# Kernel tuning notes

Hardware: AMD Instinct MI355X
Metric: run time of the kernel (lower is better)

The kernel has to match this reference:

```python
import math
import jax, jax.numpy as jnp
import numpy as np

NUM_HEADS = 8
C_HIDDEN = 32
C_Q = 64
C_KV = 64
INF = 1.0e9


def setup_inputs() -> dict:
    key = jax.random.key(0)
    ks = jax.random.split(key, 8)
    B, S, Q, KV = 1, 128, 256, 256
    H, D = NUM_HEADS, C_HIDDEN
    input_q = jax.random.normal(ks[0], (B, S, Q, C_Q), dtype=jnp.float32)
    input_kv = jax.random.normal(ks[1], (B, S, KV, C_KV), dtype=jnp.float32)
    mask = jnp.ones((B, S, 1, 1, KV), dtype=jnp.float32)
    bias = jax.random.normal(ks[2], (B, 1, H, Q, KV), dtype=jnp.float32)
    # Glorot-ish init for projections
    wq = jax.random.normal(ks[3], (C_Q, H * D), dtype=jnp.float32) * (1.0 / math.sqrt(C_Q))
    wk = jax.random.normal(ks[4], (C_KV, H * D), dtype=jnp.float32) * (1.0 / math.sqrt(C_KV))
    wv = jax.random.normal(ks[5], (C_KV, H * D), dtype=jnp.float32) * (1.0 / math.sqrt(C_KV))
    wo = jax.random.normal(ks[6], (H * D, C_Q), dtype=jnp.float32) * (1.0 / math.sqrt(H * D))
    bo = jnp.zeros((C_Q,), dtype=jnp.float32)
    return {"input_q": input_q, "input_kv": input_kv, "mask": mask, "bias": bias,
            "wq": wq, "wk": wk, "wv": wv, "wo": wo, "bo": bo}


def _split_heads(x):
    # [..., L, H*D] -> [..., H, L, D]
    *lead, L, HD = x.shape
    x = x.reshape(*lead, L, NUM_HEADS, C_HIDDEN)
    return jnp.swapaxes(x, -2, -3)


def reference(input_q, input_kv, mask, bias, wq, wk, wv, wo, bo):
    q = _split_heads(input_q @ wq)   # [B,S,H,Q,D]
    k = _split_heads(input_kv @ wk)  # [B,S,H,KV,D]
    v = _split_heads(input_kv @ wv)  # [B,S,H,KV,D]
    scaling = 1.0 / math.sqrt(C_HIDDEN)
    a = jnp.einsum("bshqd,bshkd->bshqk", q * scaling, k)
    a = a + (mask - 1.0) * INF + bias
    a = jax.nn.softmax(a, axis=-1)
    o = jnp.einsum("bshqk,bshkd->bshqd", a, v)
    o = jnp.swapaxes(o, -2, -3)  # [B,S,Q,H,D]
    o = o.reshape(o.shape[:-2] + (NUM_HEADS * C_HIDDEN,))
    return o @ wo + bo
```

## Files before the change

kernel.cpp:

```cpp
#include <hip/hip_runtime.h>

typedef __bf16 bf16_t;
typedef __bf16 bf16x4_t __attribute__((ext_vector_type(4)));
typedef __bf16 bf16x8 __attribute__((ext_vector_type(8)));
typedef float f32x4 __attribute__((ext_vector_type(4)));

#define NH 8
#define DH 32
#define QL 256
#define KL 256
#define CIN 64
#define HD 256

__device__ __forceinline__ bf16_t f2bf(float x) { return (bf16_t)x; }

__device__ __forceinline__ f32x4 mfma16(bf16x8 a, bf16x8 b, f32x4 c) {
    return __builtin_amdgcn_mfma_f32_16x16x32_bf16(a, b, c, 0, 0, 0);
}

__launch_bounds__(256)
__global__ void pack_w(const float* __restrict__ Wq, const float* __restrict__ Wk,
                       const float* __restrict__ Wv, const float* __restrict__ Wo,
                       bf16_t* __restrict__ WqF, bf16_t* __restrict__ WkF,
                       bf16_t* __restrict__ WvF, bf16_t* __restrict__ WoF) {
    const int h = blockIdx.x;
    const int tid = threadIdx.x, lane = tid & 63, w = tid >> 6;
    const int quad = lane >> 4, l16 = lane & 15;
    if (w < 3) {
        const float* __restrict__ W = (w == 0) ? Wq : (w == 1 ? Wk : Wv);
        bf16_t* __restrict__ F = (w == 0) ? WqF : (w == 1 ? WkF : WvF);
#pragma unroll
        for (int nt = 0; nt < 2; ++nt)
#pragma unroll
            for (int ks = 0; ks < 2; ++ks) {
                bf16x8 f;
#pragma unroll
                for (int j = 0; j < 8; ++j)
                    f[j] = f2bf(W[(ks * 32 + quad * 8 + j) * HD + h * DH + nt * 16 + l16]);
                *(bf16x8*)&F[(size_t)((h * 4 + nt * 2 + ks) * 512) + lane * 8] = f;
            }
    } else {
#pragma unroll
        for (int nt = 0; nt < 4; ++nt) {
            bf16x8 f;
#pragma unroll
            for (int j = 0; j < 8; ++j)
                f[j] = f2bf(Wo[(h * DH + quad * 8 + j) * CIN + nt * 16 + l16]);
            *(bf16x8*)&WoF[(size_t)((h * 4 + nt) * 512) + lane * 8] = f;
        }
    }
}

__launch_bounds__(256, 3)
__global__ void fused_sb(const float* __restrict__ Xq, const float* __restrict__ Xkv,
                         const float* __restrict__ Mask, const float* __restrict__ Bias,
                         const bf16_t* __restrict__ WqF, const bf16_t* __restrict__ WkF,
                         const bf16_t* __restrict__ WvF, const bf16_t* __restrict__ WoF,
                         const float* __restrict__ Bo, float* __restrict__ Out) {
    const int b = blockIdx.x;
    const int s = b & 127;
    const int qq = (b >> 7) & 3, hg = b >> 9;
    const int tid = threadIdx.x, lane = tid & 63, w = tid >> 6;
    const int quad = lane >> 4, l16 = lane & 15;
    const int tg = qq * 4 + w;
    const f32x4 vzero = {0.f, 0.f, 0.f, 0.f};

    __shared__ __attribute__((aligned(16))) bf16_t sK[KL * 32];
    __shared__ __attribute__((aligned(16))) bf16_t sVT[DH][264];
    __shared__ __attribute__((aligned(16))) bf16_t sPT[4][16][72];
    __shared__ __attribute__((aligned(16))) float sMask[KL];

    if (tid < 64) {
        const f32x4 m4 = *(const f32x4*)&Mask[s * KL + tid * 4];
        f32x4 mm;
#pragma unroll
        for (int j = 0; j < 4; ++j) mm[j] = (m4[j] - 1.0f) * 1.0e9f;
        *(f32x4*)&sMask[tid * 4] = mm;
    }

    bf16x8 xk[4][2];
#pragma unroll
    for (int t = 0; t < 4; ++t) {
        const int row = (w * 4 + t) * 16 + l16;
        const float* src = &Xkv[(size_t)(s * QL + row) * CIN];
#pragma unroll
        for (int ks = 0; ks < 2; ++ks) {
            const f32x4 lo = *(const f32x4*)&src[ks * 32 + quad * 8];
            const f32x4 hi = *(const f32x4*)&src[ks * 32 + quad * 8 + 4];
            bf16x8 f;
#pragma unroll
            for (int j = 0; j < 4; ++j) { f[j] = f2bf(lo[j]); f[4 + j] = f2bf(hi[j]); }
            xk[t][ks] = f;
        }
    }
    bf16x8 xq[2];
    {
        const int row = tg * 16 + l16;
        const float* src = &Xq[(size_t)(s * QL + row) * CIN];
#pragma unroll
        for (int ks = 0; ks < 2; ++ks) {
            const f32x4 lo = *(const f32x4*)&src[ks * 32 + quad * 8];
            const f32x4 hi = *(const f32x4*)&src[ks * 32 + quad * 8 + 4];
            bf16x8 f;
#pragma unroll
            for (int j = 0; j < 4; ++j) {
                f[j] = f2bf(lo[j] * 0.17677669529663687f);
                f[4 + j] = f2bf(hi[j] * 0.17677669529663687f);
            }
            xq[ks] = f;
        }
    }

    auto projK = [&](int h) {
        bf16x8 bk[2][2];
#pragma unroll
        for (int nt = 0; nt < 2; ++nt)
#pragma unroll
            for (int ks = 0; ks < 2; ++ks)
                bk[nt][ks] = *(const bf16x8*)&WkF[(size_t)((h * 4 + nt * 2 + ks) * 512) + lane * 8];
#pragma unroll
        for (int t = 0; t < 4; ++t) {
            const int r0 = (w * 4 + t) * 16 + quad * 4;
#pragma unroll
            for (int nt = 0; nt < 2; ++nt) {
                f32x4 c = mfma16(xk[t][0], bk[nt][0], vzero);
                c = mfma16(xk[t][1], bk[nt][1], c);
                const int chS = ((nt * 2 + (l16 >> 3)) ^ quad) << 3;
#pragma unroll
                for (int r = 0; r < 4; ++r)
                    sK[(r0 + r) * 32 + chS + (l16 & 7)] = f2bf(c[r]);
            }
        }
    };
    auto projV = [&](int h) {
        bf16x8 bv[2][2];
#pragma unroll
        for (int nt = 0; nt < 2; ++nt)
#pragma unroll
            for (int ks = 0; ks < 2; ++ks)
                bv[nt][ks] = *(const bf16x8*)&WvF[(size_t)((h * 4 + nt * 2 + ks) * 512) + lane * 8];
#pragma unroll
        for (int t = 0; t < 4; ++t) {
            const int c0 = (w * 4 + t) * 16 + quad * 4;
#pragma unroll
            for (int nt = 0; nt < 2; ++nt) {
                f32x4 c = mfma16(xk[t][0], bv[nt][0], vzero);
                c = mfma16(xk[t][1], bv[nt][1], c);
                bf16x4_t p4;
#pragma unroll
                for (int r = 0; r < 4; ++r) p4[r] = f2bf(c[r]);
                *(bf16x4_t*)&sVT[nt * 16 + l16][c0] = p4;
            }
        }
    };
    auto projQ = [&](int h) -> bf16x8 {
        bf16x8 bq[2][2];
#pragma unroll
        for (int nt = 0; nt < 2; ++nt)
#pragma unroll
            for (int ks = 0; ks < 2; ++ks)
                bq[nt][ks] = *(const bf16x8*)&WqF[(size_t)((h * 4 + nt * 2 + ks) * 512) + lane * 8];
#pragma unroll
        for (int nt = 0; nt < 2; ++nt) {
            f32x4 c = mfma16(xq[0], bq[nt][0], vzero);
            c = mfma16(xq[1], bq[nt][1], c);
#pragma unroll
            for (int r = 0; r < 4; ++r) sPT[w][quad * 4 + r][nt * 16 + l16] = f2bf(c[r]);
        }
        return *(const bf16x8*)&sPT[w][l16][quad * 8];
    };

    f32x4 acc[4];
#pragma unroll
    for (int nt = 0; nt < 4; ++nt) acc[nt] = vzero;

    f32x4 sv[16];
    {
        const float* bb = &Bias[(size_t)(hg * 4 * QL + tg * 16 + l16) * KL];
#pragma unroll
        for (int ct = 0; ct < 16; ++ct) sv[ct] = *(const f32x4*)&bb[ct * 16 + quad * 4];
    }
    projK(hg * 4);
    projV(hg * 4);
    bf16x8 qfr = projQ(hg * 4);
    __syncthreads();

#pragma unroll 1
    for (int hh = 0; hh < 4; ++hh) {
        const int h = hg * 4 + hh;

#pragma unroll
        for (int ct = 0; ct < 16; ++ct) {
            const int row = ct * 16 + l16;
            const int chS = (quad ^ ((l16 >> 2) & 3)) << 3;
            const bf16x8 ak = *(const bf16x8*)&sK[row * 32 + chS];
            sv[ct] = mfma16(ak, qfr, sv[ct]);
        }

        __syncthreads();

        if (hh < 3) projK(h + 1);

#pragma unroll
        for (int ct = 0; ct < 16; ++ct)
            sv[ct] += *(const f32x4*)&sMask[ct * 16 + quad * 4];
        f32x4 vmx = sv[0];
#pragma unroll
        for (int ct = 1; ct < 16; ++ct)
#pragma unroll
            for (int r = 0; r < 4; ++r) vmx[r] = fmaxf(vmx[r], sv[ct][r]);
        float mx = fmaxf(fmaxf(vmx[0], vmx[1]), fmaxf(vmx[2], vmx[3]));
        mx = fmaxf(mx, __shfl_xor(mx, 16, 64));
        mx = fmaxf(mx, __shfl_xor(mx, 32, 64));
        f32x4 vsum = vzero;
#pragma unroll
        for (int ct = 0; ct < 16; ++ct)
#pragma unroll
            for (int r = 0; r < 4; ++r) {
                const float e = __expf(sv[ct][r] - mx);
                sv[ct][r] = e;
                vsum[r] += e;
            }
        float sum = (vsum[0] + vsum[1]) + (vsum[2] + vsum[3]);
        sum += __shfl_xor(sum, 16, 64);
        sum += __shfl_xor(sum, 32, 64);
        const float rs = 1.0f / sum;

        f32x4 o0 = vzero, o1 = vzero;
#pragma unroll
        for (int c = 0; c < 4; ++c) {
#pragma unroll
            for (int cc = 0; cc < 4; ++cc) {
                const int ct = c * 4 + cc;
                bf16x4_t pv;
#pragma unroll
                for (int r = 0; r < 4; ++r) pv[r] = f2bf(sv[ct][r] * rs);
                *(bf16x4_t*)&sPT[w][l16][cc * 16 + quad * 4] = pv;
            }
#pragma unroll
            for (int ks = 0; ks < 2; ++ks) {
                const bf16x8 ap = *(const bf16x8*)&sPT[w][l16][ks * 32 + quad * 8];
                const int cs = c * 2 + ks;
                const bf16x8 v0 = *(const bf16x8*)&sVT[l16][cs * 32 + quad * 8];
                const bf16x8 v1 = *(const bf16x8*)&sVT[16 + l16][cs * 32 + quad * 8];
                o0 = mfma16(ap, v0, o0);
                o1 = mfma16(ap, v1, o1);
            }
        }

        __syncthreads();

        if (hh < 3) projV(h + 1);

        {
            bf16x8 bwo[4];
#pragma unroll
            for (int nt = 0; nt < 4; ++nt)
                bwo[nt] = *(const bf16x8*)&WoF[(size_t)((h * 4 + nt) * 512) + lane * 8];
#pragma unroll
            for (int r = 0; r < 4; ++r) {
                sPT[w][quad * 4 + r][l16] = f2bf(o0[r]);
                sPT[w][quad * 4 + r][16 + l16] = f2bf(o1[r]);
            }
            const bf16x8 af = *(const bf16x8*)&sPT[w][l16][quad * 8];
#pragma unroll
            for (int nt = 0; nt < 4; ++nt) acc[nt] = mfma16(af, bwo[nt], acc[nt]);
        }

        if (hh < 3) {
            qfr = projQ(h + 1);
            const float* bb = &Bias[(size_t)((h + 1) * QL + tg * 16 + l16) * KL];
#pragma unroll
            for (int ct = 0; ct < 16; ++ct) sv[ct] = *(const f32x4*)&bb[ct * 16 + quad * 4];
        }
    }

    const int orow = s * QL + tg * 16 + quad * 4;
#pragma unroll
    for (int nt = 0; nt < 4; ++nt) {
        const float bo = (hg == 0) ? Bo[nt * 16 + l16] : 0.0f;
#pragma unroll
        for (int r = 0; r < 4; ++r)
            atomicAdd(&Out[(size_t)(orow + r) * CIN + nt * 16 + l16], acc[nt][r] + bo);
    }
}

extern "C" void kernel_launch(void* const* d_in, const int* in_sizes, int n_in,
                              void* d_out, int out_size, void* d_ws, size_t ws_size,
                              hipStream_t stream) {
    const float* Xq   = (const float*)d_in[0];
    const float* Xkv  = (const float*)d_in[1];
    const float* Mask = (const float*)d_in[2];
    const float* Bias = (const float*)d_in[3];
    const float* Wq   = (const float*)d_in[4];
    const float* Wk   = (const float*)d_in[5];
    const float* Wv   = (const float*)d_in[6];
    const float* Wo   = (const float*)d_in[7];
    const float* Bo   = (const float*)d_in[8];
    float* Out = (float*)d_out;

    bf16_t* WqF = (bf16_t*)d_ws;
    bf16_t* WkF = WqF + 16384;
    bf16_t* WvF = WkF + 16384;
    bf16_t* WoF = WvF + 16384;

    pack_w<<<dim3(NH), 256, 0, stream>>>(Wq, Wk, Wv, Wo, WqF, WkF, WvF, WoF);
    hipMemsetAsync(d_out, 0, (size_t)out_size, stream);
    fused_sb<<<dim3(1024), 256, 0, stream>>>(Xq, Xkv, Mask, Bias,
                                             WqF, WkF, WvF, WoF, Bo, Out);
}
```

Before: 158.9 us.

## Process all heads per block, two heads interleaved, replacing atomics with plain stores

The head-group split across blocks is removed, so each block now covers all 8 heads for its (s, q-tile) and the grid halves to 512 blocks. Heads are handled in pairs with double-buffered K/V shared memory, which gives two independent MFMA and softmax chains to interleave for more ILP. Because one block owns a full output tile, the memset and the atomicAdd output accumulation are replaced by direct stores. The cost is more registers and LDS per block, lower occupancy (launch bound 2 instead of 3), and half as many blocks, which may under-fill the GPU's compute units and repeats the X loads less often but spends more serial time per block.

```diff
diff --git a/kernel.cpp b/kernel.cpp
--- a/kernel.cpp
+++ b/kernel.cpp
@@ -51,22 +51,21 @@
     }
 }
 
-__launch_bounds__(256, 3)
-__global__ void fused_sb(const float* __restrict__ Xq, const float* __restrict__ Xkv,
+__launch_bounds__(256, 2)
+__global__ void fused_g2(const float* __restrict__ Xq, const float* __restrict__ Xkv,
                          const float* __restrict__ Mask, const float* __restrict__ Bias,
                          const bf16_t* __restrict__ WqF, const bf16_t* __restrict__ WkF,
                          const bf16_t* __restrict__ WvF, const bf16_t* __restrict__ WoF,
                          const float* __restrict__ Bo, float* __restrict__ Out) {
     const int b = blockIdx.x;
-    const int s = b & 127;
-    const int qq = (b >> 7) & 3, hg = b >> 9;
+    const int s = b & 127, qq = b >> 7;
     const int tid = threadIdx.x, lane = tid & 63, w = tid >> 6;
     const int quad = lane >> 4, l16 = lane & 15;
     const int tg = qq * 4 + w;
     const f32x4 vzero = {0.f, 0.f, 0.f, 0.f};
 
-    __shared__ __attribute__((aligned(16))) bf16_t sK[KL * 32];
-    __shared__ __attribute__((aligned(16))) bf16_t sVT[DH][264];
+    __shared__ __attribute__((aligned(16))) bf16_t sK[2][KL * 32];
+    __shared__ __attribute__((aligned(16))) bf16_t sVT[2][DH][264];
     __shared__ __attribute__((aligned(16))) bf16_t sPT[4][16][72];
     __shared__ __attribute__((aligned(16))) float sMask[KL];
 
@@ -111,7 +110,7 @@
         }
     }
 
-    auto projK = [&](int h) {
+    auto projK = [&](int h, int buf) {
         bf16x8 bk[2][2];
 #pragma unroll
         for (int nt = 0; nt < 2; ++nt)
@@ -128,11 +127,11 @@
                 const int chS = ((nt * 2 + (l16 >> 3)) ^ quad) << 3;
 #pragma unroll
                 for (int r = 0; r < 4; ++r)
-                    sK[(r0 + r) * 32 + chS + (l16 & 7)] = f2bf(c[r]);
+                    sK[buf][(r0 + r) * 32 + chS + (l16 & 7)] = f2bf(c[r]);
             }
         }
     };
-    auto projV = [&](int h) {
+    auto projV = [&](int h, int buf) {
         bf16x8 bv[2][2];
 #pragma unroll
         for (int nt = 0; nt < 2; ++nt)
@@ -149,7 +148,7 @@
                 bf16x4_t p4;
 #pragma unroll
                 for (int r = 0; r < 4; ++r) p4[r] = f2bf(c[r]);
-                *(bf16x4_t*)&sVT[nt * 16 + l16][c0] = p4;
+                *(bf16x4_t*)&sVT[buf][nt * 16 + l16][c0] = p4;
             }
         }
     };
@@ -174,59 +173,89 @@
 #pragma unroll
     for (int nt = 0; nt < 4; ++nt) acc[nt] = vzero;
 
-    f32x4 sv[16];
-    {
-        const float* bb = &Bias[(size_t)(hg * 4 * QL + tg * 16 + l16) * KL];
-#pragma unroll
-        for (int ct = 0; ct < 16; ++ct) sv[ct] = *(const f32x4*)&bb[ct * 16 + quad * 4];
-    }
-    projK(hg * 4);
-    projV(hg * 4);
-    bf16x8 qfr = projQ(hg * 4);
+    f32x4 sv[2][16];
+#pragma unroll
+    for (int u = 0; u < 2; ++u) {
+        const float* bb = &Bias[(size_t)(u * QL + tg * 16 + l16) * KL];
+#pragma unroll
+        for (int ct = 0; ct < 16; ++ct) sv[u][ct] = *(const f32x4*)&bb[ct * 16 + quad * 4];
+    }
+    projK(0, 0);
+    projK(1, 1);
+    projV(0, 0);
+    projV(1, 1);
+    bf16x8 qfr0 = projQ(0);
+    bf16x8 qfr1 = projQ(1);
     __syncthreads();
 
 #pragma unroll 1
-    for (int hh = 0; hh < 4; ++hh) {
-        const int h = hg * 4 + hh;
+    for (int i = 0; i < 4; ++i) {
+        const int h0 = 2 * i, h1 = 2 * i + 1;
 
 #pragma unroll
         for (int ct = 0; ct < 16; ++ct) {
             const int row = ct * 16 + l16;
             const int chS = (quad ^ ((l16 >> 2) & 3)) << 3;
-            const bf16x8 ak = *(const bf16x8*)&sK[row * 32 + chS];
-            sv[ct] = mfma16(ak, qfr, sv[ct]);
+            const bf16x8 ak0 = *(const bf16x8*)&sK[0][row * 32 + chS];
+            const bf16x8 ak1 = *(const bf16x8*)&sK[1][row * 32 + chS];
+            sv[0][ct] = mfma16(ak0, qfr0, sv[0][ct]);
+            sv[1][ct] = mfma16(ak1, qfr1, sv[1][ct]);
         }
 
         __syncthreads();
 
-        if (hh < 3) projK(h + 1);
-
+        if (i < 3) {
+            projK(h0 + 2, 0);
+            projK(h1 + 2, 1);
+        }
+
+        f32x4 vmx0, vmx1;
+        {
+            const f32x4 m0 = *(const f32x4*)&sMask[0 * 16 + quad * 4];
+            sv[0][0] += m0;
+            sv[1][0] += m0;
+            vmx0 = sv[0][0];
+            vmx1 = sv[1][0];
+        }
+#pragma unroll
+        for (int ct = 1; ct < 16; ++ct) {
+            const f32x4 mm = *(const f32x4*)&sMask[ct * 16 + quad * 4];
+            sv[0][ct] += mm;
+            sv[1][ct] += mm;
+#pragma unroll
+            for (int r = 0; r < 4; ++r) {
+                vmx0[r] = fmaxf(vmx0[r], sv[0][ct][r]);
+                vmx1[r] = fmaxf(vmx1[r], sv[1][ct][r]);
+            }
+        }
+        float mx0 = fmaxf(fmaxf(vmx0[0], vmx0[1]), fmaxf(vmx0[2], vmx0[3]));
+        float mx1 = fmaxf(fmaxf(vmx1[0], vmx1[1]), fmaxf(vmx1[2], vmx1[3]));
+        mx0 = fmaxf(mx0, __shfl_xor(mx0, 16, 64));
+        mx1 = fmaxf(mx1, __shfl_xor(mx1, 16, 64));
+        mx0 = fmaxf(mx0, __shfl_xor(mx0, 32, 64));
+        mx1 = fmaxf(mx1, __shfl_xor(mx1, 32, 64));
+        f32x4 vs0 = vzero, vs1 = vzero;
 #pragma unroll
         for (int ct = 0; ct < 16; ++ct)
-            sv[ct] += *(const f32x4*)&sMask[ct * 16 + quad * 4];
-        f32x4 vmx = sv[0];
-#pragma unroll
-        for (int ct = 1; ct < 16; ++ct)
-#pragma unroll
-            for (int r = 0; r < 4; ++r) vmx[r] = fmaxf(vmx[r], sv[ct][r]);
-        float mx = fmaxf(fmaxf(vmx[0], vmx[1]), fmaxf(vmx[2], vmx[3]));
-        mx = fmaxf(mx, __shfl_xor(mx, 16, 64));
-        mx = fmaxf(mx, __shfl_xor(mx, 32, 64));
-        f32x4 vsum = vzero;
-#pragma unroll
-        for (int ct = 0; ct < 16; ++ct)
 #pragma unroll
             for (int r = 0; r < 4; ++r) {
-                const float e = __expf(sv[ct][r] - mx);
-                sv[ct][r] = e;
-                vsum[r] += e;
-            }
-        float sum = (vsum[0] + vsum[1]) + (vsum[2] + vsum[3]);
-        sum += __shfl_xor(sum, 16, 64);
-        sum += __shfl_xor(sum, 32, 64);
-        const float rs = 1.0f / sum;
-
-        f32x4 o0 = vzero, o1 = vzero;
+                const float e0 = __expf(sv[0][ct][r] - mx0);
+                const float e1 = __expf(sv[1][ct][r] - mx1);
+                sv[0][ct][r] = e0;
+                sv[1][ct][r] = e1;
+                vs0[r] += e0;
+                vs1[r] += e1;
+            }
+        float sum0 = (vs0[0] + vs0[1]) + (vs0[2] + vs0[3]);
+        float sum1 = (vs1[0] + vs1[1]) + (vs1[2] + vs1[3]);
+        sum0 += __shfl_xor(sum0, 16, 64);
+        sum1 += __shfl_xor(sum1, 16, 64);
+        sum0 += __shfl_xor(sum0, 32, 64);
+        sum1 += __shfl_xor(sum1, 32, 64);
+        const float rs0 = 1.0f / sum0;
+        const float rs1 = 1.0f / sum1;
+
+        f32x4 o00 = vzero, o01 = vzero, o10 = vzero, o11 = vzero;
 #pragma unroll
         for (int c = 0; c < 4; ++c) {
 #pragma unroll
@@ -234,54 +263,93 @@
                 const int ct = c * 4 + cc;
                 bf16x4_t pv;
 #pragma unroll
-                for (int r = 0; r < 4; ++r) pv[r] = f2bf(sv[ct][r] * rs);
+                for (int r = 0; r < 4; ++r) pv[r] = f2bf(sv[0][ct][r] * rs0);
                 *(bf16x4_t*)&sPT[w][l16][cc * 16 + quad * 4] = pv;
             }
 #pragma unroll
             for (int ks = 0; ks < 2; ++ks) {
                 const bf16x8 ap = *(const bf16x8*)&sPT[w][l16][ks * 32 + quad * 8];
                 const int cs = c * 2 + ks;
-                const bf16x8 v0 = *(const bf16x8*)&sVT[l16][cs * 32 + quad * 8];
-                const bf16x8 v1 = *(const bf16x8*)&sVT[16 + l16][cs * 32 + quad * 8];
-                o0 = mfma16(ap, v0, o0);
-                o1 = mfma16(ap, v1, o1);
+                const bf16x8 v0 = *(const bf16x8*)&sVT[0][l16][cs * 32 + quad * 8];
+                const bf16x8 v1 = *(const bf16x8*)&sVT[0][16 + l16][cs * 32 + quad * 8];
+                o00 = mfma16(ap, v0, o00);
+                o01 = mfma16(ap, v1, o01);
+            }
+#pragma unroll
+            for (int cc = 0; cc < 4; ++cc) {
+                const int ct = c * 4 + cc;
+                bf16x4_t pv;
+#pragma unroll
+                for (int r = 0; r < 4; ++r) pv[r] = f2bf(sv[1][ct][r] * rs1);
+                *(bf16x4_t*)&sPT[w][l16][cc * 16 + quad * 4] = pv;
+            }
+#pragma unroll
+            for (int ks = 0; ks < 2; ++ks) {
+                const bf16x8 ap = *(const bf16x8*)&sPT[w][l16][ks * 32 + quad * 8];
+                const int cs = c * 2 + ks;
+                const bf16x8 v0 = *(const bf16x8*)&sVT[1][l16][cs * 32 + quad * 8];
+                const bf16x8 v1 = *(const bf16x8*)&sVT[1][16 + l16][cs * 32 + quad * 8];
+                o10 = mfma16(ap, v0, o10);
+                o11 = mfma16(ap, v1, o11);
             }
         }
 
         __syncthreads();
 
-        if (hh < 3) projV(h + 1);
+        if (i < 3) {
+            projV(h0 + 2, 0);
+            projV(h1 + 2, 1);
+        }
 
         {
             bf16x8 bwo[4];
 #pragma unroll
             for (int nt = 0; nt < 4; ++nt)
-                bwo[nt] = *(const bf16x8*)&WoF[(size_t)((h * 4 + nt) * 512) + lane * 8];
+                bwo[nt] = *(const bf16x8*)&WoF[(size_t)((h0 * 4 + nt) * 512) + lane * 8];
 #pragma unroll
             for (int r = 0; r < 4; ++r) {
-                sPT[w][quad * 4 + r][l16] = f2bf(o0[r]);
-                sPT[w][quad * 4 + r][16 + l16] = f2bf(o1[r]);
+                sPT[w][quad * 4 + r][l16] = f2bf(o00[r]);
+                sPT[w][quad * 4 + r][16 + l16] = f2bf(o01[r]);
             }
             const bf16x8 af = *(const bf16x8*)&sPT[w][l16][quad * 8];
 #pragma unroll
             for (int nt = 0; nt < 4; ++nt) acc[nt] = mfma16(af, bwo[nt], acc[nt]);
         }
-
-        if (hh < 3) {
-            qfr = projQ(h + 1);
-            const float* bb = &Bias[(size_t)((h + 1) * QL + tg * 16 + l16) * KL];
-#pragma unroll
-            for (int ct = 0; ct < 16; ++ct) sv[ct] = *(const f32x4*)&bb[ct * 16 + quad * 4];
+        {
+            bf16x8 bwo[4];
+#pragma unroll
+            for (int nt = 0; nt < 4; ++nt)
+                bwo[nt] = *(const bf16x8*)&WoF[(size_t)((h1 * 4 + nt) * 512) + lane * 8];
+#pragma unroll
+            for (int r = 0; r < 4; ++r) {
+                sPT[w][quad * 4 + r][l16] = f2bf(o10[r]);
+                sPT[w][quad * 4 + r][16 + l16] = f2bf(o11[r]);
+            }
+            const bf16x8 af = *(const bf16x8*)&sPT[w][l16][quad * 8];
+#pragma unroll
+            for (int nt = 0; nt < 4; ++nt) acc[nt] = mfma16(af, bwo[nt], acc[nt]);
+        }
+
+        if (i < 3) {
+            qfr0 = projQ(h0 + 2);
+            qfr1 = projQ(h1 + 2);
+#pragma unroll
+            for (int u = 0; u < 2; ++u) {
+                const float* bb = &Bias[(size_t)((h0 + 2 + u) * QL + tg * 16 + l16) * KL];
+#pragma unroll
+                for (int ct = 0; ct < 16; ++ct)
+                    sv[u][ct] = *(const f32x4*)&bb[ct * 16 + quad * 4];
+            }
         }
     }
 
     const int orow = s * QL + tg * 16 + quad * 4;
 #pragma unroll
     for (int nt = 0; nt < 4; ++nt) {
-        const float bo = (hg == 0) ? Bo[nt * 16 + l16] : 0.0f;
+        const float bo = Bo[nt * 16 + l16];
 #pragma unroll
         for (int r = 0; r < 4; ++r)
-            atomicAdd(&Out[(size_t)(orow + r) * CIN + nt * 16 + l16], acc[nt][r] + bo);
+            Out[(size_t)(orow + r) * CIN + nt * 16 + l16] = acc[nt][r] + bo;
     }
 }
 
@@ -305,7 +373,6 @@
     bf16_t* WoF = WvF + 16384;
 
     pack_w<<<dim3(NH), 256, 0, stream>>>(Wq, Wk, Wv, Wo, WqF, WkF, WvF, WoF);
-    hipMemsetAsync(d_out, 0, (size_t)out_size, stream);
-    fused_sb<<<dim3(1024), 256, 0, stream>>>(Xq, Xkv, Mask, Bias,
-                                             WqF, WkF, WvF, WoF, Bo, Out);
+    fused_g2<<<dim3(512), 256, 0, stream>>>(Xq, Xkv, Mask, Bias,
+                                            WqF, WkF, WvF, WoF, Bo, Out);
 }
```

Result: faster. 148.9 us (-6.3%).
